# Kernel tuning notes

Hardware: AMD Instinct MI355X
Metric: run time of the kernel (lower is better)

Reference implementation:

```python
import jax, jax.numpy as jnp
import numpy as np

L, E, H = 4, 512, 8          # layers, embed_dim, heads
V, TD, A = 16, 6, 3          # num_vocab, tree_depth, spatial_dim
N, S = 2, 1024               # batch, seq_len
D = E // H                   # head dim
FF = 4 * E                   # ffn dim

def _ln(x, g, b):
    m = jnp.mean(x, axis=-1, keepdims=True)
    v = jnp.mean((x - m) ** 2, axis=-1, keepdims=True)
    return (x - m) * jax.lax.rsqrt(v + 1e-5) * g + b

def setup_inputs() -> dict:
    key = jax.random.key(0)
    ks = iter(jax.random.split(key, 48))
    nrm = lambda shape, s=0.02: jax.random.normal(next(ks), shape, jnp.float32) * s
    inp = {}
    inp["seq"] = jax.random.randint(next(ks), (N, S), 0, V + 1)
    inp["depth"] = jax.random.randint(next(ks), (N, S), 0, TD + 1)
    inp["pos"] = jax.random.randint(next(ks), (A, N, S), 0, 2 ** TD + 1)
    # embeddings with padding_idx=0 rows zeroed
    inp["tok_emb"] = nrm((V + 1, E)).at[0].set(0.0)
    inp["depth_emb"] = nrm((TD + 1, E)).at[0].set(0.0)
    inp["sp_emb"] = nrm((A, 2 ** TD + 1, E)).at[:, 0].set(0.0)
    inp["sos"] = nrm((E,), 1.0)
    inp["Wq"] = nrm((L, E, E)); inp["bq"] = jnp.zeros((L, E))
    inp["Wk"] = nrm((L, E, E)); inp["bk"] = jnp.zeros((L, E))
    inp["Wv"] = nrm((L, E, E)); inp["bv"] = jnp.zeros((L, E))
    inp["Wo"] = nrm((L, E, E)); inp["bo"] = jnp.zeros((L, E))
    inp["g1"] = jnp.ones((L, E)); inp["b1"] = jnp.zeros((L, E))
    inp["W1"] = nrm((L, FF, E)); inp["bf1"] = jnp.zeros((L, FF))
    inp["W2"] = nrm((L, E, FF)); inp["bf2"] = jnp.zeros((L, E))
    inp["g2"] = jnp.ones((L, E)); inp["b2"] = jnp.zeros((L, E))
    inp["gf"] = jnp.ones((E,)); inp["bfin"] = jnp.zeros((E,))
    inp["Whead"] = nrm((V + 1, E))
    return inp

def reference(seq, depth, pos, tok_emb, depth_emb, sp_emb, sos, Wq, bq, Wk, bk, Wv, bv, Wo, bo, g1, b1, W1, bf1, W2, bf2, g2, b2, gf, bfin, Whead):
    n, s = seq.shape
    mask = (seq != 0).astype(jnp.float32)  # padding length-mask, applied to keys [N,S]
    # summed embeddings
    x = tok_emb[seq] + depth_emb[depth]
    for a in range(pos.shape[0]):  # spatial_dim=3, fixed small loop
        x = x + sp_emb[a][pos[a]]
    # shift right with learned SOS token
    x = jnp.concatenate([jnp.broadcast_to(sos, (n, 1, E)), x[:, :-1, :]], axis=1)
    for l in range(Wq.shape[0]):  # fixed num_layers
        # --- causal linear attention (fast-transformers 'causal-linear') ---
        q = (x @ Wq[l].T + bq[l]).reshape(n, s, H, D)
        k = (x @ Wk[l].T + bk[l]).reshape(n, s, H, D)
        v = (x @ Wv[l].T + bv[l]).reshape(n, s, H, D)
        Qf = jax.nn.elu(q) + 1.0                               # elu feature map
        Kf = (jax.nn.elu(k) + 1.0) * mask[:, :, None, None]    # zero padded keys
        # causal recurrence via cumulative sums of k (x) v outer products
        kv = jnp.cumsum(jnp.einsum('nshd,nshm->nshdm', Kf, v), axis=1)  # [N,S,H,D,D]
        Z = 1.0 / (jnp.einsum('nshd,nshd->nsh', Qf, jnp.cumsum(Kf, axis=1)) + 1e-6)
        att = (jnp.einsum('nshd,nshdm->nshm', Qf, kv) * Z[..., None]).reshape(n, s, E)
        x = x + att @ Wo[l].T + bo[l]
        x = _ln(x, g1[l], b1[l])
        # --- GELU FFN (post-norm, fast-transformers TransformerEncoderLayer) ---
        y = jax.nn.gelu(x @ W1[l].T + bf1[l], approximate=False)
        y = y @ W2[l].T + bf2[l]
        x = _ln(x + y, g2[l], b2[l])
    x = _ln(x, gf, bfin)  # final encoder LayerNorm (builder default)
    return x @ Whead.T    # logits [N,S,V+1]
```

## Files before the change

kernel.cpp:

```cpp
#include <hip/hip_runtime.h>
#include <hip/hip_bf16.h>

#define NB 2
#define SS 1024
#define EE 512
#define HH 8
#define DD 64
#define LL 4
#define FFD 2048
#define VO 17
#define MM (NB*SS)
#define CH 64
#define NCH (SS/CH)
#define NHH (NB*HH)
#define PD 68

typedef __attribute__((ext_vector_type(8))) short bshort8;
typedef __attribute__((ext_vector_type(4))) float f32x4;
typedef unsigned short u16;

__device__ __forceinline__ float b2f(u16 u) {
    return __uint_as_float(((unsigned)u) << 16);
}
__device__ __forceinline__ u16 f2b(float f) {
    unsigned u = __float_as_uint(f);
    u += 0x7fffu + ((u >> 16) & 1u);
    return (u16)(u >> 16);
}

__global__ __launch_bounds__(256) void f2b_all(
    const float* __restrict__ Wq, const float* __restrict__ Wk,
    const float* __restrict__ Wv, const float* __restrict__ Wo,
    const float* __restrict__ W1, const float* __restrict__ W2,
    u16* __restrict__ dq, u16* __restrict__ dk, u16* __restrict__ dv,
    u16* __restrict__ do_, u16* __restrict__ d1, u16* __restrict__ d2)
{
    int b = blockIdx.x;
    const float* src; u16* dst; size_t off;
    if (b < 2048) {
        int r = b >> 9, o = b & 511;
        src = (r==0)?Wq:(r==1)?Wk:(r==2)?Wv:Wo;
        dst = (r==0)?dq:(r==1)?dk:(r==2)?dv:do_;
        off = (size_t)o * 2048;
    } else {
        int bb = b - 2048;
        int r = bb >> 11, o = bb & 2047;
        src = r ? W2 : W1;
        dst = r ? d2 : d1;
        off = (size_t)o * 2048;
    }
    size_t i = off + (size_t)threadIdx.x * 8;
    float4 v0 = *(const float4*)(src + i);
    float4 v1 = *(const float4*)(src + i + 4);
    bshort8 rr;
    rr[0]=(short)f2b(v0.x); rr[1]=(short)f2b(v0.y); rr[2]=(short)f2b(v0.z); rr[3]=(short)f2b(v0.w);
    rr[4]=(short)f2b(v1.x); rr[5]=(short)f2b(v1.y); rr[6]=(short)f2b(v1.z); rr[7]=(short)f2b(v1.w);
    *(bshort8*)(dst + i) = rr;
}

__global__ __launch_bounds__(256) void embed_kernel(
    const int* __restrict__ seq, const int* __restrict__ dep,
    const int* __restrict__ pos, const float* __restrict__ tok,
    const float* __restrict__ dem, const float* __restrict__ sp,
    const float* __restrict__ sos, float* __restrict__ xf, u16* __restrict__ xh,
    float* __restrict__ mask)
{
    int m = blockIdx.x;
    int s = m % SS;
    int t = threadIdx.x;
    if (t == 0) mask[m] = (seq[m] != 0) ? 1.0f : 0.0f;
    if (s == 0) {
        for (int e = t; e < EE; e += 256) {
            float v = sos[e];
            xf[(size_t)m*EE+e] = v; xh[(size_t)m*EE+e] = f2b(v);
        }
    } else {
        int mp = m - 1;
        int tk = seq[mp];
        int dh = dep[mp];
        int p0 = pos[0*NB*SS+mp], p1 = pos[1*NB*SS+mp], p2 = pos[2*NB*SS+mp];
        const float* r0 = tok + (size_t)tk*EE;
        const float* r1 = dem + (size_t)dh*EE;
        const float* r2 = sp + ((size_t)0*65 + p0)*EE;
        const float* r3 = sp + ((size_t)1*65 + p1)*EE;
        const float* r4 = sp + ((size_t)2*65 + p2)*EE;
        for (int e = t; e < EE; e += 256) {
            float v = r0[e] + r1[e] + r2[e] + r3[e] + r4[e];
            xf[(size_t)m*EE+e] = v; xh[(size_t)m*EE+e] = f2b(v);
        }
    }
}

template<int ACT, int MODE>
__device__ __forceinline__ void gemm_body(
    const u16* __restrict__ A, const u16* __restrict__ W,
    int Kstride, int KL, const float* __restrict__ bias,
    u16* __restrict__ Ch, float* __restrict__ Cf,
    int m0, int n0, int Nn)
{
    __shared__ u16 sA[2][64][72];
    __shared__ u16 sB[2][64][72];
    int t = threadIdx.x;
    int lane = t & 63, w = t >> 6, wr = w >> 1, wc = w & 1;
    int l15 = lane & 15, lk = (lane >> 4) << 3;
    int sr = t >> 2, sc = (t & 3) << 4;
    const u16* Ap = A + (size_t)(m0 + sr) * Kstride + sc;
    const u16* Wp = W + (size_t)(n0 + sr) * Kstride + sc;
    int T = KL >> 6;
    bshort8 ra0 = *(const bshort8*)(Ap);
    bshort8 ra1 = *(const bshort8*)(Ap + 8);
    bshort8 rb0 = *(const bshort8*)(Wp);
    bshort8 rb1 = *(const bshort8*)(Wp + 8);
    *(bshort8*)&sA[0][sr][sc]   = ra0;  *(bshort8*)&sA[0][sr][sc+8] = ra1;
    *(bshort8*)&sB[0][sr][sc]   = rb0;  *(bshort8*)&sB[0][sr][sc+8] = rb1;
    __syncthreads();
    f32x4 acc[2][2] = {};
    for (int tt = 0; tt < T; ++tt) {
        int cur = tt & 1;
        bool more = (tt + 1 < T);
        if (more) {
            int kk = (tt + 1) << 6;
            ra0 = *(const bshort8*)(Ap + kk);
            ra1 = *(const bshort8*)(Ap + kk + 8);
            rb0 = *(const bshort8*)(Wp + kk);
            rb1 = *(const bshort8*)(Wp + kk + 8);
        }
        #pragma unroll
        for (int ks = 0; ks < 2; ++ks) {
            bshort8 af[2], bfr[2];
            #pragma unroll
            for (int mi=0;mi<2;++mi)
                af[mi] = *(const bshort8*)&sA[cur][wr*32+mi*16+l15][(ks<<5)+lk];
            #pragma unroll
            for (int ni=0;ni<2;++ni)
                bfr[ni] = *(const bshort8*)&sB[cur][wc*32+ni*16+l15][(ks<<5)+lk];
            #pragma unroll
            for (int mi=0;mi<2;++mi)
                #pragma unroll
                for (int ni=0;ni<2;++ni)
                    acc[mi][ni] = __builtin_amdgcn_mfma_f32_16x16x32_bf16(
                        af[mi], bfr[ni], acc[mi][ni], 0, 0, 0);
        }
        if (more) {
            int nxt = cur ^ 1;
            *(bshort8*)&sA[nxt][sr][sc]   = ra0;  *(bshort8*)&sA[nxt][sr][sc+8] = ra1;
            *(bshort8*)&sB[nxt][sr][sc]   = rb0;  *(bshort8*)&sB[nxt][sr][sc+8] = rb1;
            __syncthreads();
        }
    }
    int r0 = (lane >> 4) << 2;
    #pragma unroll
    for (int mi=0;mi<2;++mi) {
        #pragma unroll
        for (int ni=0;ni<2;++ni) {
            int col = n0 + wc*32 + ni*16 + l15;
            float bs = (MODE == 0) ? bias[col] : 0.f;
            #pragma unroll
            for (int r=0;r<4;++r) {
                int row = m0 + wr*32 + mi*16 + r0 + r;
                float v = acc[mi][ni][r] + bs;
                if (ACT == 1) v = 0.5f * v * (1.0f + erff(v * 0.70710678118654752f));
                if (MODE == 0) Ch[(size_t)row*Nn + col] = f2b(v);
                else           Cf[(size_t)row*Nn + col] = v;
            }
        }
    }
}

template<int ACT>
__global__ __launch_bounds__(256) void gemm_k(
    const u16* __restrict__ A, const u16* __restrict__ W,
    const float* __restrict__ bias, u16* __restrict__ Ch, int Nn, int K)
{
    gemm_body<ACT,0>(A, W, K, K, bias, Ch, nullptr, blockIdx.y*64, blockIdx.x*64, Nn);
}

__global__ __launch_bounds__(256) void gemm_part(
    const u16* __restrict__ A, const u16* __restrict__ W,
    float* __restrict__ P, int Nn, int Kfull, int KL)
{
    int z = blockIdx.z;
    gemm_body<0,2>(A + (size_t)z*KL, W + (size_t)z*KL, Kfull, KL, nullptr,
                   nullptr, P + (size_t)z*MM*Nn, blockIdx.y*64, blockIdx.x*64, Nn);
}

__global__ __launch_bounds__(256) void gemm_qkv(
    const u16* __restrict__ A,
    const u16* __restrict__ Wq, const u16* __restrict__ Wk, const u16* __restrict__ Wv,
    const float* __restrict__ bq, const float* __restrict__ bk, const float* __restrict__ bv,
    u16* __restrict__ qb, u16* __restrict__ kb, u16* __restrict__ vb, int Nn, int K)
{
    int z = blockIdx.z;
    const u16* W = (z==0) ? Wq : (z==1 ? Wk : Wv);
    const float* bias = (z==0) ? bq : (z==1 ? bk : bv);
    u16* Ch = (z==0) ? qb : (z==1 ? kb : vb);
    gemm_body<0,0>(A, W, K, K, bias, Ch, nullptr, blockIdx.y*64, blockIdx.x*64, Nn);
}

__global__ __launch_bounds__(256) void gemm_head(
    const float* __restrict__ A, const float* __restrict__ W,
    float* __restrict__ C, int M, int Nn, int K)
{
    __shared__ float sA[16][64];
    __shared__ float sB[16][64];
    int t = threadIdx.x;
    int tx = t & 15, ty = t >> 4;
    int m0 = blockIdx.y * 64, n0 = blockIdx.x * 64;
    int lr = t >> 2;
    int lc = (t & 3) << 2;
    const float* Ap = A + (size_t)(m0+lr)*K + lc;
    const float* Wp = (n0+lr < Nn) ? (W + (size_t)(n0+lr)*K + lc) : nullptr;
    float acc[4][4] = {};
    for (int kk = 0; kk < K; kk += 16) {
        float4 a4 = *(const float4*)(Ap + kk);
        float4 b4 = Wp ? *(const float4*)(Wp + kk) : make_float4(0.f,0.f,0.f,0.f);
        __syncthreads();
        sA[lc+0][lr]=a4.x; sA[lc+1][lr]=a4.y; sA[lc+2][lr]=a4.z; sA[lc+3][lr]=a4.w;
        sB[lc+0][lr]=b4.x; sB[lc+1][lr]=b4.y; sB[lc+2][lr]=b4.z; sB[lc+3][lr]=b4.w;
        __syncthreads();
        #pragma unroll
        for (int k = 0; k < 16; ++k) {
            float4 av = *(const float4*)&sA[k][ty<<2];
            float4 bv = *(const float4*)&sB[k][tx<<2];
            float aa[4] = {av.x, av.y, av.z, av.w};
            float bb[4] = {bv.x, bv.y, bv.z, bv.w};
            #pragma unroll
            for (int i=0;i<4;++i)
                #pragma unroll
                for (int j=0;j<4;++j)
                    acc[i][j] = fmaf(aa[i], bb[j], acc[i][j]);
        }
    }
    #pragma unroll
    for (int i=0;i<4;++i) {
        int mr = m0 + (ty<<2) + i;
        #pragma unroll
        for (int j=0;j<4;++j) {
            int nc = n0 + (tx<<2) + j;
            if (nc < Nn) C[(size_t)mr*Nn + nc] = acc[i][j];
        }
    }
}

__global__ __launch_bounds__(256) void attn_kv(
    const u16* __restrict__ kbuf, const u16* __restrict__ vbuf,
    const float* __restrict__ mask, float* __restrict__ kvc, float* __restrict__ zsum)
{
    int c = blockIdx.x, nh = blockIdx.y;
    int n = nh >> 3, h = nh & 7;
    __shared__ float sK[64][PD];
    __shared__ float sV[64][PD];
    int t = threadIdx.x;
    for (int idx = t; idx < 4096; idx += 256) {
        int i = idx >> 6, d = idx & 63;
        int m = n*SS + c*64 + i;
        float kk = b2f(kbuf[(size_t)m*EE + h*DD + d]);
        float f = kk > 0.f ? kk + 1.f : expf(kk);
        sK[i][d] = f * mask[m];
        sV[i][d] = b2f(vbuf[(size_t)m*EE + h*DD + d]);
    }
    __syncthreads();
    int tr = t >> 4, tc = t & 15;
    float acc[4][4] = {};
    for (int i = 0; i < 64; ++i) {
        float4 kd = *(const float4*)&sK[i][tr<<2];
        float4 vm = *(const float4*)&sV[i][tc<<2];
        float ka[4]={kd.x,kd.y,kd.z,kd.w}, vv[4]={vm.x,vm.y,vm.z,vm.w};
        #pragma unroll
        for (int a=0;a<4;++a)
            #pragma unroll
            for (int b=0;b<4;++b)
                acc[a][b] = fmaf(ka[a], vv[b], acc[a][b]);
    }
    size_t base = ((size_t)nh*NCH + c) * 4096;
    #pragma unroll
    for (int a=0;a<4;++a)
        *(float4*)&kvc[base + (size_t)((tr<<2)+a)*64 + (tc<<2)] =
            make_float4(acc[a][0],acc[a][1],acc[a][2],acc[a][3]);
    if (t < 64) {
        float z = 0.f;
        for (int i = 0; i < 64; ++i) z += sK[i][t];
        zsum[((size_t)nh*NCH + c)*64 + t] = z;
    }
}

__global__ __launch_bounds__(256) void attn_prefix(
    float* __restrict__ kvc, float* __restrict__ zsum)
{
    int s = blockIdx.x, nh = blockIdx.y;
    int t = threadIdx.x;
    int idx = s * 256 + t;
    size_t base = (size_t)nh * NCH * 4096 + idx;
    float v[NCH];
    #pragma unroll
    for (int c = 0; c < NCH; ++c) v[c] = kvc[base + (size_t)c*4096];
    float run = 0.f;
    #pragma unroll
    for (int c = 0; c < NCH; ++c) {
        kvc[base + (size_t)c*4096] = run;
        run += v[c];
    }
    if (s == 0 && t < 64) {
        size_t zb = (size_t)nh * NCH * 64 + t;
        float zv[NCH];
        #pragma unroll
        for (int c = 0; c < NCH; ++c) zv[c] = zsum[zb + (size_t)c*64];
        float zr = 0.f;
        #pragma unroll
        for (int c = 0; c < NCH; ++c) {
            zsum[zb + (size_t)c*64] = zr;
            zr += zv[c];
        }
    }
}

__global__ __launch_bounds__(256) void attn_out(
    const u16* __restrict__ qbuf, const u16* __restrict__ kbuf,
    const u16* __restrict__ vbuf, const float* __restrict__ mask,
    const float* __restrict__ stc, const float* __restrict__ zpref,
    u16* __restrict__ att)
{
    int c = blockIdx.x, nh = blockIdx.y;
    int n = nh >> 3, h = nh & 7;
    __shared__ float sQ[64][PD], sK[64][PD], sV[64][PD], sP[64][PD];
    __shared__ float sZ[64], sInv[64];
    __shared__ float sDen[64][4];
    int t = threadIdx.x;
    for (int idx = t; idx < 4096; idx += 256) {
        int i = idx >> 6, d = idx & 63;
        int m = n*SS + c*64 + i;
        float qq = b2f(qbuf[(size_t)m*EE + h*DD + d]);
        sQ[i][d] = qq > 0.f ? qq + 1.f : expf(qq);
        float kk = b2f(kbuf[(size_t)m*EE + h*DD + d]);
        float f = kk > 0.f ? kk + 1.f : expf(kk);
        sK[i][d] = f * mask[m];
        sV[i][d] = b2f(vbuf[(size_t)m*EE + h*DD + d]);
    }
    if (t < 64) sZ[t] = zpref[((size_t)nh*NCH + c)*64 + t];
    __syncthreads();
    int tr = t >> 4, tc = t & 15;
    {
        float acc[4][4] = {};
        for (int d = 0; d < 64; d += 4) {
            float4 qa[4], kb4[4];
            #pragma unroll
            for (int a=0;a<4;++a) qa[a] = *(const float4*)&sQ[(tr<<2)+a][d];
            #pragma unroll
            for (int b=0;b<4;++b) kb4[b] = *(const float4*)&sK[(tc<<2)+b][d];
            #pragma unroll
            for (int a=0;a<4;++a) {
                float qv[4] = {qa[a].x,qa[a].y,qa[a].z,qa[a].w};
                #pragma unroll
                for (int b=0;b<4;++b) {
                    acc[a][b] += qv[0]*kb4[b].x + qv[1]*kb4[b].y
                               + qv[2]*kb4[b].z + qv[3]*kb4[b].w;
                }
            }
        }
        #pragma unroll
        for (int a=0;a<4;++a)
            *(float4*)&sP[(tr<<2)+a][tc<<2] =
                make_float4(acc[a][0],acc[a][1],acc[a][2],acc[a][3]);
    }
    __syncthreads();
    {
        size_t sb = ((size_t)nh*NCH + c) * 4096;
        for (int idx = t; idx < 4096; idx += 256)
            sK[idx>>6][idx&63] = stc[sb + idx];
    }
    {
        int rr = t & 63, qq = t >> 6;
        int j0 = qq << 4;
        float part = 0.f;
        #pragma unroll
        for (int j = 0; j < 16; ++j) {
            int jj = j0 + j;
            part += (jj <= rr) ? sP[rr][jj] : 0.f;
        }
        float dzp = 0.f;
        #pragma unroll
        for (int d = 0; d < 16; ++d) {
            int dd = j0 + d;
            dzp += sQ[rr][dd] * sZ[dd];
        }
        sDen[rr][qq] = part + dzp;
    }
    float acc1[4][4] = {};
    for (int j = 0; j < 64; ++j) {
        float4 vb4 = *(const float4*)&sV[j][tc<<2];
        float vv[4] = {vb4.x, vb4.y, vb4.z, vb4.w};
        #pragma unroll
        for (int a=0;a<4;++a) {
            int i = (tr<<2)+a;
            float p = (j <= i) ? sP[i][j] : 0.f;
            #pragma unroll
            for (int b=0;b<4;++b) acc1[a][b] = fmaf(p, vv[b], acc1[a][b]);
        }
    }
    __syncthreads();
    if (t < 64)
        sInv[t] = 1.0f / (1e-6f + sDen[t][0] + sDen[t][1] + sDen[t][2] + sDen[t][3]);
    for (int d = 0; d < 64; ++d) {
        float4 sv4 = *(const float4*)&sK[d][tc<<2];
        float sv[4] = {sv4.x, sv4.y, sv4.z, sv4.w};
        #pragma unroll
        for (int a=0;a<4;++a) {
            float qv = sQ[(tr<<2)+a][d];
            #pragma unroll
            for (int b=0;b<4;++b) acc1[a][b] = fmaf(qv, sv[b], acc1[a][b]);
        }
    }
    __syncthreads();
    #pragma unroll
    for (int a=0;a<4;++a) {
        int i = (tr<<2)+a;
        int m = n*SS + c*64 + i;
        float inv = sInv[i];
        size_t ob = (size_t)m*EE + h*DD + (tc<<2);
        att[ob+0] = f2b(acc1[a][0]*inv);
        att[ob+1] = f2b(acc1[a][1]*inv);
        att[ob+2] = f2b(acc1[a][2]*inv);
        att[ob+3] = f2b(acc1[a][3]*inv);
    }
}

__global__ __launch_bounds__(256) void ln_kernel(
    const float* __restrict__ in, const float* __restrict__ g,
    const float* __restrict__ b, float* __restrict__ outf)
{
    int m = blockIdx.x;
    int t = threadIdx.x;
    float v0 = in[(size_t)m*EE + t];
    float v1 = in[(size_t)m*EE + t + 256];
    float s = v0 + v1, sq = v0*v0 + v1*v1;
    for (int o = 32; o; o >>= 1) { s += __shfl_down(s, o); sq += __shfl_down(sq, o); }
    __shared__ float ws_[4], wq_[4];
    int w = t >> 6;
    if ((t & 63) == 0) { ws_[w] = s; wq_[w] = sq; }
    __syncthreads();
    if (t == 0) {
        float S=0.f, Q=0.f;
        for (int i=0;i<4;++i){S+=ws_[i];Q+=wq_[i];}
        float mean = S * (1.0f/512.0f);
        float var = Q * (1.0f/512.0f) - mean*mean;
        ws_[0] = mean; wq_[0] = rsqrtf(var + 1e-5f);
    }
    __syncthreads();
    float mean = ws_[0], inv = wq_[0];
    outf[(size_t)m*EE + t]       = (v0-mean)*inv*g[t]+b[t];
    outf[(size_t)m*EE + t + 256] = (v1-mean)*inv*g[t+256]+b[t+256];
}

__global__ __launch_bounds__(256) void ln_fuse2(
    const float* __restrict__ p0, const float* __restrict__ p1,
    const float* __restrict__ bias, const float* __restrict__ resid,
    const float* __restrict__ g, const float* __restrict__ b,
    float* __restrict__ outf, u16* __restrict__ outh)
{
    int m = blockIdx.x;
    int t = threadIdx.x;
    size_t i0 = (size_t)m*EE + t, i1 = i0 + 256;
    float v0 = p0[i0] + p1[i0] + bias[t]     + resid[i0];
    float v1 = p0[i1] + p1[i1] + bias[t+256] + resid[i1];
    float s = v0 + v1, sq = v0*v0 + v1*v1;
    for (int o = 32; o; o >>= 1) { s += __shfl_down(s, o); sq += __shfl_down(sq, o); }
    __shared__ float ws_[4], wq_[4];
    int w = t >> 6;
    if ((t & 63) == 0) { ws_[w] = s; wq_[w] = sq; }
    __syncthreads();
    if (t == 0) {
        float S=0.f, Q=0.f;
        for (int i=0;i<4;++i){S+=ws_[i];Q+=wq_[i];}
        float mean = S * (1.0f/512.0f);
        float var = Q * (1.0f/512.0f) - mean*mean;
        ws_[0] = mean; wq_[0] = rsqrtf(var + 1e-5f);
    }
    __syncthreads();
    float mean = ws_[0], inv = wq_[0];
    float o0 = (v0-mean)*inv*g[t]+b[t];
    float o1 = (v1-mean)*inv*g[t+256]+b[t+256];
    outf[i0] = o0;  outf[i1] = o1;
    outh[i0] = f2b(o0);  outh[i1] = f2b(o1);
}

extern "C" void kernel_launch(void* const* d_in, const int* in_sizes, int n_in,
                              void* d_out, int out_size, void* d_ws, size_t ws_size,
                              hipStream_t stream)
{
    (void)in_sizes; (void)n_in; (void)out_size; (void)ws_size;
    const int*   seq = (const int*)d_in[0];
    const int*   dep = (const int*)d_in[1];
    const int*   pos = (const int*)d_in[2];
    const float* tok = (const float*)d_in[3];
    const float* dem = (const float*)d_in[4];
    const float* sp  = (const float*)d_in[5];
    const float* sos = (const float*)d_in[6];
    const float* Wq  = (const float*)d_in[7];
    const float* bq  = (const float*)d_in[8];
    const float* Wk  = (const float*)d_in[9];
    const float* bk  = (const float*)d_in[10];
    const float* Wv  = (const float*)d_in[11];
    const float* bv  = (const float*)d_in[12];
    const float* Wo  = (const float*)d_in[13];
    const float* bo  = (const float*)d_in[14];
    const float* g1  = (const float*)d_in[15];
    const float* b1  = (const float*)d_in[16];
    const float* W1  = (const float*)d_in[17];
    const float* bf1 = (const float*)d_in[18];
    const float* W2  = (const float*)d_in[19];
    const float* bf2 = (const float*)d_in[20];
    const float* g2  = (const float*)d_in[21];
    const float* b2  = (const float*)d_in[22];
    const float* gf  = (const float*)d_in[23];
    const float* bfn = (const float*)d_in[24];
    const float* Wh  = (const float*)d_in[25];
    float* out = (float*)d_out;

    float* xf    = (float*)d_ws;
    float* yb    = xf   + (size_t)MM*EE;
    float* kvc   = yb   + (size_t)MM*EE;
    float* zsum  = kvc  + (size_t)NHH*NCH*DD*DD;
    float* maskb = zsum + (size_t)NHH*NCH*DD;
    float* part  = maskb + MM;
    u16* xh   = (u16*)(part + (size_t)2*MM*EE);
    u16* qb   = xh + (size_t)MM*EE;
    u16* kb   = qb + (size_t)MM*EE;
    u16* vb   = kb + (size_t)MM*EE;
    u16* attb = vb + (size_t)MM*EE;
    u16* h1   = qb;
    u16* wq16 = attb + (size_t)MM*EE;
    u16* wk16 = wq16 + (size_t)LL*EE*EE;
    u16* wv16 = wk16 + (size_t)LL*EE*EE;
    u16* wo16 = wv16 + (size_t)LL*EE*EE;
    u16* w116 = wo16 + (size_t)LL*EE*EE;
    u16* w216 = w116 + (size_t)LL*FFD*EE;

    dim3 blk(256);
    dim3 gQKV(EE/64, MM/64, 3);
    dim3 gF(FFD/64, MM/64);
    dim3 gS(EE/64,  MM/64, 2);
    dim3 gA(NCH, NHH);
    dim3 gP(NCH, NHH);

    f2b_all<<<6144, blk, 0, stream>>>(Wq, Wk, Wv, Wo, W1, W2,
                                      wq16, wk16, wv16, wo16, w116, w216);
    embed_kernel<<<MM, blk, 0, stream>>>(seq, dep, pos, tok, dem, sp, sos, xf, xh, maskb);
    for (int l = 0; l < LL; ++l) {
        gemm_qkv<<<gQKV, blk, 0, stream>>>(
            xh, wq16 + (size_t)l*EE*EE, wk16 + (size_t)l*EE*EE, wv16 + (size_t)l*EE*EE,
            bq + (size_t)l*EE, bk + (size_t)l*EE, bv + (size_t)l*EE,
            qb, kb, vb, EE, EE);
        attn_kv<<<gA, blk, 0, stream>>>(kb, vb, maskb, kvc, zsum);
        attn_prefix<<<gP, blk, 0, stream>>>(kvc, zsum);
        attn_out<<<gA, blk, 0, stream>>>(qb, kb, vb, maskb, kvc, zsum, attb);
        gemm_part<<<gS, blk, 0, stream>>>(attb, wo16 + (size_t)l*EE*EE, part, EE, EE, EE/2);
        ln_fuse2<<<MM, blk, 0, stream>>>(part, part + (size_t)MM*EE, bo + (size_t)l*EE,
                                         xf, g1 + (size_t)l*EE, b1 + (size_t)l*EE, xf, xh);
        gemm_k<1><<<gF, blk, 0, stream>>>(xh, w116 + (size_t)l*FFD*EE,
                                          bf1 + (size_t)l*FFD, h1, FFD, EE);
        gemm_part<<<gS, blk, 0, stream>>>(h1, w216 + (size_t)l*EE*FFD, part, EE, FFD, FFD/2);
        ln_fuse2<<<MM, blk, 0, stream>>>(part, part + (size_t)MM*EE, bf2 + (size_t)l*EE,
                                         xf, g2 + (size_t)l*EE, b2 + (size_t)l*EE, xf, xh);
    }
    ln_kernel<<<MM, blk, 0, stream>>>(xf, gf, bfn, yb);
    gemm_head<<<dim3(1, MM/64), blk, 0, stream>>>(yb, Wh, out, MM, VO, EE);
}
```

Baseline: 484.5 us.

## Deepen GEMM global-load prefetch and use 4-way split-K for Wo/W2 projections

The GEMM main loop now keeps two k-tiles in flight in registers (two register sets, loop unrolled by two) instead of one. This hides more global-memory latency at the cost of extra VGPRs. The Wo and W2 projection GEMMs move from a 2-way to a 4-way split-K, doubling their block count for better CU occupancy on small grids. The LayerNorm fusion kernel now sums four partial buffers, which adds partial-sum traffic and workspace.

```diff
diff --git a/kernel.cpp b/kernel.cpp
--- a/kernel.cpp
+++ b/kernel.cpp
@@ -107,47 +107,47 @@
     const u16* Ap = A + (size_t)(m0 + sr) * Kstride + sc;
     const u16* Wp = W + (size_t)(n0 + sr) * Kstride + sc;
     int T = KL >> 6;
-    bshort8 ra0 = *(const bshort8*)(Ap);
-    bshort8 ra1 = *(const bshort8*)(Ap + 8);
-    bshort8 rb0 = *(const bshort8*)(Wp);
-    bshort8 rb1 = *(const bshort8*)(Wp + 8);
-    *(bshort8*)&sA[0][sr][sc]   = ra0;  *(bshort8*)&sA[0][sr][sc+8] = ra1;
-    *(bshort8*)&sB[0][sr][sc]   = rb0;  *(bshort8*)&sB[0][sr][sc+8] = rb1;
-    __syncthreads();
+    bshort8 a0_0, a1_0, b0_0, b1_0;
+    bshort8 a0_1, a1_1, b0_1, b1_1;
+
+#define GB_LOAD0(KK) { a0_0 = *(const bshort8*)(Ap + (KK)); a1_0 = *(const bshort8*)(Ap + (KK) + 8); \
+                       b0_0 = *(const bshort8*)(Wp + (KK)); b1_0 = *(const bshort8*)(Wp + (KK) + 8); }
+#define GB_LOAD1(KK) { a0_1 = *(const bshort8*)(Ap + (KK)); a1_1 = *(const bshort8*)(Ap + (KK) + 8); \
+                       b0_1 = *(const bshort8*)(Wp + (KK)); b1_1 = *(const bshort8*)(Wp + (KK) + 8); }
+#define GB_WRITE0(BUF) { *(bshort8*)&sA[BUF][sr][sc] = a0_0; *(bshort8*)&sA[BUF][sr][sc+8] = a1_0; \
+                         *(bshort8*)&sB[BUF][sr][sc] = b0_0; *(bshort8*)&sB[BUF][sr][sc+8] = b1_0; }
+#define GB_WRITE1(BUF) { *(bshort8*)&sA[BUF][sr][sc] = a0_1; *(bshort8*)&sA[BUF][sr][sc+8] = a1_1; \
+                         *(bshort8*)&sB[BUF][sr][sc] = b0_1; *(bshort8*)&sB[BUF][sr][sc+8] = b1_1; }
+#define GB_COMPUTE(BUF) { _Pragma("unroll") for (int ks = 0; ks < 2; ++ks) { \
+        bshort8 af[2], bfr[2]; \
+        _Pragma("unroll") for (int mi=0;mi<2;++mi) af[mi] = *(const bshort8*)&sA[BUF][wr*32+mi*16+l15][(ks<<5)+lk]; \
+        _Pragma("unroll") for (int ni=0;ni<2;++ni) bfr[ni] = *(const bshort8*)&sB[BUF][wc*32+ni*16+l15][(ks<<5)+lk]; \
+        _Pragma("unroll") for (int mi=0;mi<2;++mi) { _Pragma("unroll") for (int ni=0;ni<2;++ni) \
+            acc[mi][ni] = __builtin_amdgcn_mfma_f32_16x16x32_bf16(af[mi], bfr[ni], acc[mi][ni], 0, 0, 0); } } }
+
     f32x4 acc[2][2] = {};
-    for (int tt = 0; tt < T; ++tt) {
-        int cur = tt & 1;
-        bool more = (tt + 1 < T);
-        if (more) {
-            int kk = (tt + 1) << 6;
-            ra0 = *(const bshort8*)(Ap + kk);
-            ra1 = *(const bshort8*)(Ap + kk + 8);
-            rb0 = *(const bshort8*)(Wp + kk);
-            rb1 = *(const bshort8*)(Wp + kk + 8);
-        }
-        #pragma unroll
-        for (int ks = 0; ks < 2; ++ks) {
-            bshort8 af[2], bfr[2];
-            #pragma unroll
-            for (int mi=0;mi<2;++mi)
-                af[mi] = *(const bshort8*)&sA[cur][wr*32+mi*16+l15][(ks<<5)+lk];
-            #pragma unroll
-            for (int ni=0;ni<2;++ni)
-                bfr[ni] = *(const bshort8*)&sB[cur][wc*32+ni*16+l15][(ks<<5)+lk];
-            #pragma unroll
-            for (int mi=0;mi<2;++mi)
-                #pragma unroll
-                for (int ni=0;ni<2;++ni)
-                    acc[mi][ni] = __builtin_amdgcn_mfma_f32_16x16x32_bf16(
-                        af[mi], bfr[ni], acc[mi][ni], 0, 0, 0);
-        }
-        if (more) {
-            int nxt = cur ^ 1;
-            *(bshort8*)&sA[nxt][sr][sc]   = ra0;  *(bshort8*)&sA[nxt][sr][sc+8] = ra1;
-            *(bshort8*)&sB[nxt][sr][sc]   = rb0;  *(bshort8*)&sB[nxt][sr][sc+8] = rb1;
+    GB_LOAD0(0);
+    GB_WRITE0(0);
+    GB_LOAD1(64);
+    if (T > 2) GB_LOAD0(128);
+    __syncthreads();
+    for (int tb = 0; tb < T; tb += 2) {
+        GB_COMPUTE(0);
+        GB_WRITE1(1);
+        if (tb + 3 < T) GB_LOAD1((tb + 3) << 6);
+        __syncthreads();
+        GB_COMPUTE(1);
+        if (tb + 2 < T) {
+            GB_WRITE0(0);
+            if (tb + 4 < T) GB_LOAD0((tb + 4) << 6);
             __syncthreads();
         }
     }
+#undef GB_LOAD0
+#undef GB_LOAD1
+#undef GB_WRITE0
+#undef GB_WRITE1
+#undef GB_COMPUTE
     int r0 = (lane >> 4) << 2;
     #pragma unroll
     for (int mi=0;mi<2;++mi) {
@@ -451,8 +451,8 @@
     outf[(size_t)m*EE + t + 256] = (v1-mean)*inv*g[t+256]+b[t+256];
 }
 
-__global__ __launch_bounds__(256) void ln_fuse2(
-    const float* __restrict__ p0, const float* __restrict__ p1,
+__global__ __launch_bounds__(256) void ln_fuse4(
+    const float* __restrict__ P,
     const float* __restrict__ bias, const float* __restrict__ resid,
     const float* __restrict__ g, const float* __restrict__ b,
     float* __restrict__ outf, u16* __restrict__ outh)
@@ -460,8 +460,9 @@
     int m = blockIdx.x;
     int t = threadIdx.x;
     size_t i0 = (size_t)m*EE + t, i1 = i0 + 256;
-    float v0 = p0[i0] + p1[i0] + bias[t]     + resid[i0];
-    float v1 = p0[i1] + p1[i1] + bias[t+256] + resid[i1];
+    const size_t PS = (size_t)MM*EE;
+    float v0 = (P[i0] + P[i0+PS]) + (P[i0+2*PS] + P[i0+3*PS]) + bias[t]     + resid[i0];
+    float v1 = (P[i1] + P[i1+PS]) + (P[i1+2*PS] + P[i1+3*PS]) + bias[t+256] + resid[i1];
     float s = v0 + v1, sq = v0*v0 + v1*v1;
     for (int o = 32; o; o >>= 1) { s += __shfl_down(s, o); sq += __shfl_down(sq, o); }
     __shared__ float ws_[4], wq_[4];
@@ -522,7 +523,7 @@
     float* zsum  = kvc  + (size_t)NHH*NCH*DD*DD;
     float* maskb = zsum + (size_t)NHH*NCH*DD;
     float* part  = maskb + MM;
-    u16* xh   = (u16*)(part + (size_t)2*MM*EE);
+    u16* xh   = (u16*)(part + (size_t)4*MM*EE);
     u16* qb   = xh + (size_t)MM*EE;
     u16* kb   = qb + (size_t)MM*EE;
     u16* vb   = kb + (size_t)MM*EE;
@@ -538,7 +539,7 @@
     dim3 blk(256);
     dim3 gQKV(EE/64, MM/64, 3);
     dim3 gF(FFD/64, MM/64);
-    dim3 gS(EE/64,  MM/64, 2);
+    dim3 gS4(EE/64, MM/64, 4);
     dim3 gA(NCH, NHH);
     dim3 gP(NCH, NHH);
 
@@ -553,13 +554,13 @@
         attn_kv<<<gA, blk, 0, stream>>>(kb, vb, maskb, kvc, zsum);
         attn_prefix<<<gP, blk, 0, stream>>>(kvc, zsum);
         attn_out<<<gA, blk, 0, stream>>>(qb, kb, vb, maskb, kvc, zsum, attb);
-        gemm_part<<<gS, blk, 0, stream>>>(attb, wo16 + (size_t)l*EE*EE, part, EE, EE, EE/2);
-        ln_fuse2<<<MM, blk, 0, stream>>>(part, part + (size_t)MM*EE, bo + (size_t)l*EE,
+        gemm_part<<<gS4, blk, 0, stream>>>(attb, wo16 + (size_t)l*EE*EE, part, EE, EE, EE/4);
+        ln_fuse4<<<MM, blk, 0, stream>>>(part, bo + (size_t)l*EE,
                                          xf, g1 + (size_t)l*EE, b1 + (size_t)l*EE, xf, xh);
         gemm_k<1><<<gF, blk, 0, stream>>>(xh, w116 + (size_t)l*FFD*EE,
                                           bf1 + (size_t)l*FFD, h1, FFD, EE);
-        gemm_part<<<gS, blk, 0, stream>>>(h1, w216 + (size_t)l*EE*FFD, part, EE, FFD, FFD/2);
-        ln_fuse2<<<MM, blk, 0, stream>>>(part, part + (size_t)MM*EE, bf2 + (size_t)l*EE,
+        gemm_part<<<gS4, blk, 0, stream>>>(h1, w216 + (size_t)l*EE*FFD, part, EE, FFD, FFD/4);
+        ln_fuse4<<<MM, blk, 0, stream>>>(part, bf2 + (size_t)l*EE,
                                          xf, g2 + (size_t)l*EE, b2 + (size_t)l*EE, xf, xh);
     }
     ln_kernel<<<MM, blk, 0, stream>>>(xf, gf, bfn, yb);
```

After: 508.3 us. 1.05x slower.

## Fuse init kernels, fold chunk prefix into attn_out, fuse final LN with head

Applied to the files above, without the earlier changes.

Merges the weight conversion and the embedding into one launch, and removes the separate attn_prefix kernel. attn_out now sums the preceding chunk states itself, so each block reads up to 15 chunk matrices redundantly. The final LayerNorm and the vocab-head projection become a single kernel that keeps the head weights in shared memory. The aim is to cut launch count and intermediate round trips, at the cost of redundant global reads in attn_out and a small head kernel in which only half the threads do the dot products.

```diff
diff --git a/kernel.cpp b/kernel.cpp
--- a/kernel.cpp
+++ b/kernel.cpp
@@ -28,65 +28,64 @@
     return (u16)(u >> 16);
 }
 
-__global__ __launch_bounds__(256) void f2b_all(
+__global__ __launch_bounds__(256) void init_all(
+    const int* __restrict__ seq, const int* __restrict__ dep,
+    const int* __restrict__ pos, const float* __restrict__ tok,
+    const float* __restrict__ dem, const float* __restrict__ sp,
+    const float* __restrict__ sos,
     const float* __restrict__ Wq, const float* __restrict__ Wk,
     const float* __restrict__ Wv, const float* __restrict__ Wo,
     const float* __restrict__ W1, const float* __restrict__ W2,
     u16* __restrict__ dq, u16* __restrict__ dk, u16* __restrict__ dv,
-    u16* __restrict__ do_, u16* __restrict__ d1, u16* __restrict__ d2)
+    u16* __restrict__ do_, u16* __restrict__ d1, u16* __restrict__ d2,
+    float* __restrict__ xf, u16* __restrict__ xh, float* __restrict__ mask)
 {
     int b = blockIdx.x;
-    const float* src; u16* dst; size_t off;
-    if (b < 2048) {
-        int r = b >> 9, o = b & 511;
-        src = (r==0)?Wq:(r==1)?Wk:(r==2)?Wv:Wo;
-        dst = (r==0)?dq:(r==1)?dk:(r==2)?dv:do_;
-        off = (size_t)o * 2048;
+    int t = threadIdx.x;
+    if (b < 6144) {
+        const float* src; u16* dst; size_t off;
+        if (b < 2048) {
+            int r = b >> 9, o = b & 511;
+            src = (r==0)?Wq:(r==1)?Wk:(r==2)?Wv:Wo;
+            dst = (r==0)?dq:(r==1)?dk:(r==2)?dv:do_;
+            off = (size_t)o * 2048;
+        } else {
+            int bb = b - 2048;
+            int r = bb >> 11, o = bb & 2047;
+            src = r ? W2 : W1;
+            dst = r ? d2 : d1;
+            off = (size_t)o * 2048;
+        }
+        size_t i = off + (size_t)t * 8;
+        float4 v0 = *(const float4*)(src + i);
+        float4 v1 = *(const float4*)(src + i + 4);
+        bshort8 rr;
+        rr[0]=(short)f2b(v0.x); rr[1]=(short)f2b(v0.y); rr[2]=(short)f2b(v0.z); rr[3]=(short)f2b(v0.w);
+        rr[4]=(short)f2b(v1.x); rr[5]=(short)f2b(v1.y); rr[6]=(short)f2b(v1.z); rr[7]=(short)f2b(v1.w);
+        *(bshort8*)(dst + i) = rr;
     } else {
-        int bb = b - 2048;
-        int r = bb >> 11, o = bb & 2047;
-        src = r ? W2 : W1;
-        dst = r ? d2 : d1;
-        off = (size_t)o * 2048;
-    }
-    size_t i = off + (size_t)threadIdx.x * 8;
-    float4 v0 = *(const float4*)(src + i);
-    float4 v1 = *(const float4*)(src + i + 4);
-    bshort8 rr;
-    rr[0]=(short)f2b(v0.x); rr[1]=(short)f2b(v0.y); rr[2]=(short)f2b(v0.z); rr[3]=(short)f2b(v0.w);
-    rr[4]=(short)f2b(v1.x); rr[5]=(short)f2b(v1.y); rr[6]=(short)f2b(v1.z); rr[7]=(short)f2b(v1.w);
-    *(bshort8*)(dst + i) = rr;
-}
-
-__global__ __launch_bounds__(256) void embed_kernel(
-    const int* __restrict__ seq, const int* __restrict__ dep,
-    const int* __restrict__ pos, const float* __restrict__ tok,
-    const float* __restrict__ dem, const float* __restrict__ sp,
-    const float* __restrict__ sos, float* __restrict__ xf, u16* __restrict__ xh,
-    float* __restrict__ mask)
-{
-    int m = blockIdx.x;
-    int s = m % SS;
-    int t = threadIdx.x;
-    if (t == 0) mask[m] = (seq[m] != 0) ? 1.0f : 0.0f;
-    if (s == 0) {
-        for (int e = t; e < EE; e += 256) {
-            float v = sos[e];
-            xf[(size_t)m*EE+e] = v; xh[(size_t)m*EE+e] = f2b(v);
-        }
-    } else {
-        int mp = m - 1;
-        int tk = seq[mp];
-        int dh = dep[mp];
-        int p0 = pos[0*NB*SS+mp], p1 = pos[1*NB*SS+mp], p2 = pos[2*NB*SS+mp];
-        const float* r0 = tok + (size_t)tk*EE;
-        const float* r1 = dem + (size_t)dh*EE;
-        const float* r2 = sp + ((size_t)0*65 + p0)*EE;
-        const float* r3 = sp + ((size_t)1*65 + p1)*EE;
-        const float* r4 = sp + ((size_t)2*65 + p2)*EE;
-        for (int e = t; e < EE; e += 256) {
-            float v = r0[e] + r1[e] + r2[e] + r3[e] + r4[e];
-            xf[(size_t)m*EE+e] = v; xh[(size_t)m*EE+e] = f2b(v);
+        int m = b - 6144;
+        int s = m % SS;
+        if (t == 0) mask[m] = (seq[m] != 0) ? 1.0f : 0.0f;
+        if (s == 0) {
+            for (int e = t; e < EE; e += 256) {
+                float v = sos[e];
+                xf[(size_t)m*EE+e] = v; xh[(size_t)m*EE+e] = f2b(v);
+            }
+        } else {
+            int mp = m - 1;
+            int tk = seq[mp];
+            int dh = dep[mp];
+            int p0 = pos[0*NB*SS+mp], p1 = pos[1*NB*SS+mp], p2 = pos[2*NB*SS+mp];
+            const float* r0 = tok + (size_t)tk*EE;
+            const float* r1 = dem + (size_t)dh*EE;
+            const float* r2 = sp + ((size_t)0*65 + p0)*EE;
+            const float* r3 = sp + ((size_t)1*65 + p1)*EE;
+            const float* r4 = sp + ((size_t)2*65 + p2)*EE;
+            for (int e = t; e < EE; e += 256) {
+                float v = r0[e] + r1[e] + r2[e] + r3[e] + r4[e];
+                xf[(size_t)m*EE+e] = v; xh[(size_t)m*EE+e] = f2b(v);
+            }
         }
     }
 }
@@ -197,51 +196,6 @@
     gemm_body<0,0>(A, W, K, K, bias, Ch, nullptr, blockIdx.y*64, blockIdx.x*64, Nn);
 }
 
-__global__ __launch_bounds__(256) void gemm_head(
-    const float* __restrict__ A, const float* __restrict__ W,
-    float* __restrict__ C, int M, int Nn, int K)
-{
-    __shared__ float sA[16][64];
-    __shared__ float sB[16][64];
-    int t = threadIdx.x;
-    int tx = t & 15, ty = t >> 4;
-    int m0 = blockIdx.y * 64, n0 = blockIdx.x * 64;
-    int lr = t >> 2;
-    int lc = (t & 3) << 2;
-    const float* Ap = A + (size_t)(m0+lr)*K + lc;
-    const float* Wp = (n0+lr < Nn) ? (W + (size_t)(n0+lr)*K + lc) : nullptr;
-    float acc[4][4] = {};
-    for (int kk = 0; kk < K; kk += 16) {
-        float4 a4 = *(const float4*)(Ap + kk);
-        float4 b4 = Wp ? *(const float4*)(Wp + kk) : make_float4(0.f,0.f,0.f,0.f);
-        __syncthreads();
-        sA[lc+0][lr]=a4.x; sA[lc+1][lr]=a4.y; sA[lc+2][lr]=a4.z; sA[lc+3][lr]=a4.w;
-        sB[lc+0][lr]=b4.x; sB[lc+1][lr]=b4.y; sB[lc+2][lr]=b4.z; sB[lc+3][lr]=b4.w;
-        __syncthreads();
-        #pragma unroll
-        for (int k = 0; k < 16; ++k) {
-            float4 av = *(const float4*)&sA[k][ty<<2];
-            float4 bv = *(const float4*)&sB[k][tx<<2];
-            float aa[4] = {av.x, av.y, av.z, av.w};
-            float bb[4] = {bv.x, bv.y, bv.z, bv.w};
-            #pragma unroll
-            for (int i=0;i<4;++i)
-                #pragma unroll
-                for (int j=0;j<4;++j)
-                    acc[i][j] = fmaf(aa[i], bb[j], acc[i][j]);
-        }
-    }
-    #pragma unroll
-    for (int i=0;i<4;++i) {
-        int mr = m0 + (ty<<2) + i;
-        #pragma unroll
-        for (int j=0;j<4;++j) {
-            int nc = n0 + (tx<<2) + j;
-            if (nc < Nn) C[(size_t)mr*Nn + nc] = acc[i][j];
-        }
-    }
-}
-
 __global__ __launch_bounds__(256) void attn_kv(
     const u16* __restrict__ kbuf, const u16* __restrict__ vbuf,
     const float* __restrict__ mask, float* __restrict__ kvc, float* __restrict__ zsum)
@@ -284,40 +238,10 @@
     }
 }
 
-__global__ __launch_bounds__(256) void attn_prefix(
-    float* __restrict__ kvc, float* __restrict__ zsum)
-{
-    int s = blockIdx.x, nh = blockIdx.y;
-    int t = threadIdx.x;
-    int idx = s * 256 + t;
-    size_t base = (size_t)nh * NCH * 4096 + idx;
-    float v[NCH];
-    #pragma unroll
-    for (int c = 0; c < NCH; ++c) v[c] = kvc[base + (size_t)c*4096];
-    float run = 0.f;
-    #pragma unroll
-    for (int c = 0; c < NCH; ++c) {
-        kvc[base + (size_t)c*4096] = run;
-        run += v[c];
-    }
-    if (s == 0 && t < 64) {
-        size_t zb = (size_t)nh * NCH * 64 + t;
-        float zv[NCH];
-        #pragma unroll
-        for (int c = 0; c < NCH; ++c) zv[c] = zsum[zb + (size_t)c*64];
-        float zr = 0.f;
-        #pragma unroll
-        for (int c = 0; c < NCH; ++c) {
-            zsum[zb + (size_t)c*64] = zr;
-            zr += zv[c];
-        }
-    }
-}
-
 __global__ __launch_bounds__(256) void attn_out(
     const u16* __restrict__ qbuf, const u16* __restrict__ kbuf,
     const u16* __restrict__ vbuf, const float* __restrict__ mask,
-    const float* __restrict__ stc, const float* __restrict__ zpref,
+    const float* __restrict__ kvc, const float* __restrict__ zsum,
     u16* __restrict__ att)
 {
     int c = blockIdx.x, nh = blockIdx.y;
@@ -336,7 +260,12 @@
         sK[i][d] = f * mask[m];
         sV[i][d] = b2f(vbuf[(size_t)m*EE + h*DD + d]);
     }
-    if (t < 64) sZ[t] = zpref[((size_t)nh*NCH + c)*64 + t];
+    if (t < 64) {
+        float z = 0.f;
+        size_t zb = (size_t)nh*NCH*64 + t;
+        for (int cc = 0; cc < c; ++cc) z += zsum[zb + (size_t)cc*64];
+        sZ[t] = z;
+    }
     __syncthreads();
     int tr = t >> 4, tc = t & 15;
     {
@@ -364,9 +293,12 @@
     }
     __syncthreads();
     {
-        size_t sb = ((size_t)nh*NCH + c) * 4096;
-        for (int idx = t; idx < 4096; idx += 256)
-            sK[idx>>6][idx&63] = stc[sb + idx];
+        size_t sb = (size_t)nh*NCH*4096;
+        for (int idx = t; idx < 4096; idx += 256) {
+            float s = 0.f;
+            for (int cc = 0; cc < c; ++cc) s += kvc[sb + (size_t)cc*4096 + idx];
+            sK[idx>>6][idx&63] = s;
+        }
     }
     {
         int rr = t & 63, qq = t >> 6;
@@ -424,33 +356,6 @@
     }
 }
 
-__global__ __launch_bounds__(256) void ln_kernel(
-    const float* __restrict__ in, const float* __restrict__ g,
-    const float* __restrict__ b, float* __restrict__ outf)
-{
-    int m = blockIdx.x;
-    int t = threadIdx.x;
-    float v0 = in[(size_t)m*EE + t];
-    float v1 = in[(size_t)m*EE + t + 256];
-    float s = v0 + v1, sq = v0*v0 + v1*v1;
-    for (int o = 32; o; o >>= 1) { s += __shfl_down(s, o); sq += __shfl_down(sq, o); }
-    __shared__ float ws_[4], wq_[4];
-    int w = t >> 6;
-    if ((t & 63) == 0) { ws_[w] = s; wq_[w] = sq; }
-    __syncthreads();
-    if (t == 0) {
-        float S=0.f, Q=0.f;
-        for (int i=0;i<4;++i){S+=ws_[i];Q+=wq_[i];}
-        float mean = S * (1.0f/512.0f);
-        float var = Q * (1.0f/512.0f) - mean*mean;
-        ws_[0] = mean; wq_[0] = rsqrtf(var + 1e-5f);
-    }
-    __syncthreads();
-    float mean = ws_[0], inv = wq_[0];
-    outf[(size_t)m*EE + t]       = (v0-mean)*inv*g[t]+b[t];
-    outf[(size_t)m*EE + t + 256] = (v1-mean)*inv*g[t+256]+b[t+256];
-}
-
 __global__ __launch_bounds__(256) void ln_fuse2(
     const float* __restrict__ p0, const float* __restrict__ p1,
     const float* __restrict__ bias, const float* __restrict__ resid,
@@ -481,6 +386,48 @@
     float o1 = (v1-mean)*inv*g[t+256]+b[t+256];
     outf[i0] = o0;  outf[i1] = o1;
     outh[i0] = f2b(o0);  outh[i1] = f2b(o1);
+}
+
+__global__ __launch_bounds__(256) void ln_head(
+    const float* __restrict__ xf, const float* __restrict__ gf,
+    const float* __restrict__ bfn, const float* __restrict__ Wh,
+    float* __restrict__ out)
+{
+    __shared__ float sW[VO][516];
+    __shared__ float sR[8][516];
+    __shared__ float sMean[8], sRstd[8];
+    int t = threadIdx.x;
+    int m0 = blockIdx.x * 8;
+    for (int i = t; i < VO*EE; i += 256) sW[i>>9][i&511] = Wh[i];
+    {
+        int r = t >> 5, l32 = t & 31;
+        const float* row = xf + (size_t)(m0 + r) * EE;
+        float s = 0.f, q = 0.f;
+        for (int j = l32; j < EE; j += 32) { float v = row[j]; s += v; q += v*v; }
+        for (int o = 16; o; o >>= 1) { s += __shfl_down(s, o, 32); q += __shfl_down(q, o, 32); }
+        if (l32 == 0) {
+            float mean = s * (1.0f/512.0f);
+            float var = q * (1.0f/512.0f) - mean*mean;
+            sMean[r] = mean; sRstd[r] = rsqrtf(var + 1e-5f);
+        }
+    }
+    __syncthreads();
+    for (int idx = t; idx < 8*EE; idx += 256) {
+        int rr = idx >> 9, k = idx & 511;
+        float v = xf[(size_t)(m0+rr)*EE + k];
+        sR[rr][k] = (v - sMean[rr]) * sRstd[rr] * gf[k] + bfn[k];
+    }
+    __syncthreads();
+    if (t < 8*VO) {
+        int r = t / VO, o = t % VO;
+        float acc = 0.f;
+        for (int k = 0; k < EE; k += 4) {
+            float4 a = *(const float4*)&sR[r][k];
+            float4 wv = *(const float4*)&sW[o][k];
+            acc += a.x*wv.x + a.y*wv.y + a.z*wv.z + a.w*wv.w;
+        }
+        out[(size_t)(m0+r)*VO + o] = acc;
+    }
 }
 
 extern "C" void kernel_launch(void* const* d_in, const int* in_sizes, int n_in,
@@ -517,8 +464,7 @@
     float* out = (float*)d_out;
 
     float* xf    = (float*)d_ws;
-    float* yb    = xf   + (size_t)MM*EE;
-    float* kvc   = yb   + (size_t)MM*EE;
+    float* kvc   = xf   + (size_t)MM*EE;
     float* zsum  = kvc  + (size_t)NHH*NCH*DD*DD;
     float* maskb = zsum + (size_t)NHH*NCH*DD;
     float* part  = maskb + MM;
@@ -540,18 +486,17 @@
     dim3 gF(FFD/64, MM/64);
     dim3 gS(EE/64,  MM/64, 2);
     dim3 gA(NCH, NHH);
-    dim3 gP(NCH, NHH);
-
-    f2b_all<<<6144, blk, 0, stream>>>(Wq, Wk, Wv, Wo, W1, W2,
-                                      wq16, wk16, wv16, wo16, w116, w216);
-    embed_kernel<<<MM, blk, 0, stream>>>(seq, dep, pos, tok, dem, sp, sos, xf, xh, maskb);
+
+    init_all<<<8192, blk, 0, stream>>>(seq, dep, pos, tok, dem, sp, sos,
+                                       Wq, Wk, Wv, Wo, W1, W2,
+                                       wq16, wk16, wv16, wo16, w116, w216,
+                                       xf, xh, maskb);
     for (int l = 0; l < LL; ++l) {
         gemm_qkv<<<gQKV, blk, 0, stream>>>(
             xh, wq16 + (size_t)l*EE*EE, wk16 + (size_t)l*EE*EE, wv16 + (size_t)l*EE*EE,
             bq + (size_t)l*EE, bk + (size_t)l*EE, bv + (size_t)l*EE,
             qb, kb, vb, EE, EE);
         attn_kv<<<gA, blk, 0, stream>>>(kb, vb, maskb, kvc, zsum);
-        attn_prefix<<<gP, blk, 0, stream>>>(kvc, zsum);
         attn_out<<<gA, blk, 0, stream>>>(qb, kb, vb, maskb, kvc, zsum, attb);
         gemm_part<<<gS, blk, 0, stream>>>(attb, wo16 + (size_t)l*EE*EE, part, EE, EE, EE/2);
         ln_fuse2<<<MM, blk, 0, stream>>>(part, part + (size_t)MM*EE, bo + (size_t)l*EE,
@@ -562,6 +507,5 @@
         ln_fuse2<<<MM, blk, 0, stream>>>(part, part + (size_t)MM*EE, bf2 + (size_t)l*EE,
                                          xf, g2 + (size_t)l*EE, b2 + (size_t)l*EE, xf, xh);
     }
-    ln_kernel<<<MM, blk, 0, stream>>>(xf, gf, bfn, yb);
-    gemm_head<<<dim3(1, MM/64), blk, 0, stream>>>(yb, Wh, out, MM, VO, EE);
-}
+    ln_head<<<MM/8, blk, 0, stream>>>(xf, gf, bfn, Wh, out);
+}
```

New measurement: 635.2 us. +31.1%, slower.
